# Kernel optimization log

Measured on AMD Instinct MI355X. Metric: run time of the kernel, lower is better.

## Reference

```python
import jax, jax.numpy as jnp
import numpy as np

B, L, D, N = 8, 2048, 1024, 16


def setup_inputs() -> dict:
    key = jax.random.key(0)
    ks = jax.random.split(key, 7)
    x = jax.random.normal(ks[0], (B, L, D), dtype=jnp.float32)
    # A = -rand(d_model, d_state) - 0.5  -> in (-1.5, -0.5)
    A = -jax.random.uniform(ks[1], (D, N), dtype=jnp.float32) - 0.5
    # nn.Linear(d_model, d_state, bias=False): weight [N, D]
    Wb = jax.random.normal(ks[2], (N, D), dtype=jnp.float32) / np.sqrt(D)
    C = jax.random.normal(ks[3], (D, N), dtype=jnp.float32) * 0.1
    Dp = jax.random.normal(ks[4], (D,), dtype=jnp.float32) * 0.1
    # nn.Linear(d_model, d_model): weight [D, D], bias [D]
    Wd = jax.random.normal(ks[5], (D, D), dtype=jnp.float32) / np.sqrt(D)
    bd = jax.random.normal(ks[6], (D,), dtype=jnp.float32) * 0.01
    return {"x": x, "A": A, "Wb": Wb, "C": C, "Dp": Dp, "Wd": Wd, "bd": bd}


def reference(x, A, Wb, C, Dp, Wd, bd):
    # Precompute input-dependent projections for all timesteps (batched GEMMs)
    dt = jax.nn.softplus(jnp.einsum('bld,ed->ble', x, Wd) + bd)  # [B,L,D]
    Bx = jnp.einsum('bld,nd->bln', x, Wb)                        # [B,L,N]

    def step(h, inp):
        dt_t, bx_t, x_t = inp                  # [B,D], [B,N], [B,D]
        dA = dt_t[..., None] * A               # [B,D,N]
        h = jnp.exp(dA) * h + dt_t[..., None] * bx_t[:, None, :]
        y = jnp.einsum('bdn,dn->bd', h, C) + Dp * x_t
        return h, y

    h0 = jnp.zeros((x.shape[0], A.shape[0], A.shape[1]), dtype=x.dtype)
    xs = (jnp.swapaxes(dt, 0, 1), jnp.swapaxes(Bx, 0, 1), jnp.swapaxes(x, 0, 1))
    _, ys = jax.lax.scan(step, h0, xs)         # ys: [L,B,D]
    return jnp.swapaxes(ys, 0, 1)              # [B,L,D]
```

## Files before the change

### kernel.cpp

```cpp
#include <hip/hip_runtime.h>
#include <hip/hip_bf16.h>
#include <stdint.h>

#define B_ 8
#define L_ 2048
#define D_ 1024
#define N_ 16
#define M_ (B_ * L_)
#define K_ D_
#define SEG_ 64
#define SLEN_ (L_ / SEG_)
#define LOG2E 1.44269504088896341f

typedef __bf16 bf16;
typedef __bf16 bf16x8 __attribute__((ext_vector_type(8)));
typedef float f32x4 __attribute__((ext_vector_type(4)));

__global__ __launch_bounds__(256) void cvt_f32_bf16(const float* __restrict__ in,
                                                    bf16* __restrict__ out, int n4) {
  int i = blockIdx.x * 256 + threadIdx.x;
  const int stride = gridDim.x * 256;
  const float4* in4 = (const float4*)in;
  uint2* out2 = (uint2*)out;
  for (; i < n4; i += stride) {
    float4 v = in4[i];
    union { bf16 h[4]; uint2 u; } p;
    p.h[0] = (bf16)v.x; p.h[1] = (bf16)v.y; p.h[2] = (bf16)v.z; p.h[3] = (bf16)v.w;
    out2[i] = p.u;
  }
}

__device__ inline void gload_lds16(const bf16* g, bf16* l) {
  __builtin_amdgcn_global_load_lds(
      (const __attribute__((address_space(1))) void*)g,
      (__attribute__((address_space(3))) void*)l, 16, 0, 0);
}

__device__ inline float softplus_f(float z) {
  return fmaxf(z, 0.f) + __logf(1.f + __expf(-fabsf(z)));
}

__global__ __launch_bounds__(256) void gemm_dt(const bf16* __restrict__ Xb,
                                               const bf16* __restrict__ Wdb,
                                               const float* __restrict__ bd,
                                               bf16* __restrict__ dtb) {
  __shared__ bf16 As[2][128 * 32];
  __shared__ bf16 Bs[2][128 * 32];
  const int tid = threadIdx.x;
  const int lane = tid & 63;
  const int wave = tid >> 6;
  const int wr = wave >> 1, wc = wave & 1;
  const int virt = (blockIdx.x & 7) * 128 + (blockIdx.x >> 3);
  const int mt = virt >> 3, nt = virt & 7;
  const int m0 = mt * 128, n0 = nt * 128;

  const bf16* ga[2];
  const bf16* gb[2];
#pragma unroll
  for (int q = 0; q < 2; ++q) {
    const int c = tid + 256 * q;
    const int row = c >> 2;
    const int col8 = ((c & 3) ^ (row & 3)) * 8;
    ga[q] = Xb + (size_t)(m0 + row) * K_ + col8;
    gb[q] = Wdb + (size_t)(n0 + row) * K_ + col8;
  }

  f32x4 acc[4][4] = {};
  const int frow = (lane & 15);
  const int khalf = (lane >> 4);

  int aoff[4], boff[4];
#pragma unroll
  for (int i = 0; i < 4; ++i) {
    const int Ra = wr * 64 + i * 16 + frow;
    const int Rb = wc * 64 + i * 16 + frow;
    aoff[i] = Ra * 32 + (khalf ^ (Ra & 3)) * 8;
    boff[i] = Rb * 32 + (khalf ^ (Rb & 3)) * 8;
  }

#define STAGE_(buf, kt)                                         \
  {                                                             \
    gload_lds16(ga[0] + (kt), &As[buf][tid * 8]);               \
    gload_lds16(ga[1] + (kt), &As[buf][(tid + 256) * 8]);       \
    gload_lds16(gb[0] + (kt), &Bs[buf][tid * 8]);               \
    gload_lds16(gb[1] + (kt), &Bs[buf][(tid + 256) * 8]);       \
  }

  STAGE_(0, 0);
  __syncthreads();

  int cur = 0;
  for (int t = 0; t < K_ / 32; ++t) {
    if (t + 1 < K_ / 32) STAGE_(cur ^ 1, (t + 1) * 32);
    bf16x8 af[4], bfr[4];
#pragma unroll
    for (int i = 0; i < 4; ++i) af[i] = *(const bf16x8*)&As[cur][aoff[i]];
#pragma unroll
    for (int i = 0; i < 4; ++i) bfr[i] = *(const bf16x8*)&Bs[cur][boff[i]];
#pragma unroll
    for (int i = 0; i < 4; ++i)
#pragma unroll
      for (int j = 0; j < 4; ++j)
        acc[i][j] = __builtin_amdgcn_mfma_f32_16x16x32_bf16(af[i], bfr[j], acc[i][j], 0, 0, 0);
    __syncthreads();
    cur ^= 1;
  }
#undef STAGE_

  const int rbase = m0 + wr * 64 + (lane >> 4) * 4;
  const int cbase = n0 + wc * 64 + (lane & 15);
#pragma unroll
  for (int j = 0; j < 4; ++j) {
    const int col = cbase + j * 16;
    const float bias = bd[col];
#pragma unroll
    for (int i = 0; i < 4; ++i) {
      const int row = rbase + i * 16;
#pragma unroll
      for (int r = 0; r < 4; ++r) {
        float z = acc[i][j][r] + bias;
        dtb[(size_t)(row + r) * D_ + col] = (bf16)softplus_f(z);
      }
    }
  }
}

__global__ __launch_bounds__(256) void bx_mfma(const bf16* __restrict__ Xb,
                                               const bf16* __restrict__ Wbb,
                                               float* __restrict__ Bx) {
  const int lane = threadIdx.x & 63;
  const int wave = threadIdx.x >> 6;
  const int row0 = blockIdx.x * 64 + wave * 16;
  const int fr = lane & 15;
  const int kg = (lane >> 4) * 8;
  const bf16* ga = Xb + (size_t)(row0 + fr) * K_ + kg;
  const bf16* gb = Wbb + (size_t)fr * K_ + kg;
  f32x4 acc = {};
#pragma unroll 8
  for (int kt = 0; kt < K_; kt += 32) {
    bf16x8 af = *(const bf16x8*)(ga + kt);
    bf16x8 bf = *(const bf16x8*)(gb + kt);
    acc = __builtin_amdgcn_mfma_f32_16x16x32_bf16(af, bf, acc, 0, 0, 0);
  }
  const int orow = row0 + (lane >> 4) * 4;
  const int ocol = lane & 15;
#pragma unroll
  for (int r = 0; r < 4; ++r)
    Bx[(size_t)(orow + r) * N_ + ocol] = acc[r];
}

__global__ __launch_bounds__(256) void scan_p1(
    const bf16* __restrict__ dtb, const float* __restrict__ Bx,
    const float* __restrict__ A, bf16* __restrict__ hseg,
    float* __restrict__ stot) {
  const int tid = threadIdx.x;
  const int bi = blockIdx.x;
  const int seg = bi & 63;
  const int dtile = (bi >> 6) & 3;
  const int b = bi >> 8;
  const int d = dtile * 256 + tid;
  const int l0 = seg * SLEN_;

  const float* bxp = Bx + ((size_t)b * L_ + l0) * N_;

  float A2[N_];
  {
    const float4* ap = (const float4*)(A + (size_t)d * N_);
#pragma unroll
    for (int q = 0; q < 4; ++q) {
      float4 a = ap[q];
      A2[q * 4 + 0] = a.x * LOG2E; A2[q * 4 + 1] = a.y * LOG2E;
      A2[q * 4 + 2] = a.z * LOG2E; A2[q * 4 + 3] = a.w * LOG2E;
    }
  }

  const bf16* dtp = dtb + ((size_t)b * L_ + l0) * D_ + d;
  float h[N_] = {};
  float s = 0.f;

  float cdt[4];
#pragma unroll
  for (int u = 0; u < 4; ++u) cdt[u] = (float)dtp[(size_t)u * D_];

#define P1_STEP(i, c0)                                              \
  {                                                                 \
    s += (c0);                                                      \
    _Pragma("unroll")                                               \
    for (int q = 0; q < 4; ++q) {                                   \
      const float4 bv = *(const float4*)(bxp + (i) * N_ + q * 4);   \
      const float bvf[4] = {bv.x, bv.y, bv.z, bv.w};                \
      _Pragma("unroll")                                             \
      for (int j = 0; j < 4; ++j) {                                 \
        const int n = q * 4 + j;                                    \
        const float e = __builtin_amdgcn_exp2f((c0) * A2[n]);       \
        h[n] = fmaf(e, h[n], (c0) * bvf[j]);                        \
      }                                                             \
    }                                                               \
  }

  for (int i0 = 0; i0 < SLEN_ - 4; i0 += 4) {
#pragma unroll
    for (int u = 0; u < 4; ++u) {
      const int i = i0 + u;
      const float c0 = cdt[u];
      cdt[u] = (float)dtp[(size_t)(i + 4) * D_];
      P1_STEP(i, c0);
    }
  }
#pragma unroll
  for (int u = 0; u < 4; ++u) {
    const int i = SLEN_ - 4 + u;
    P1_STEP(i, cdt[u]);
  }
#undef P1_STEP

  bf16* hp = hseg + (((size_t)b * SEG_ + seg) * D_ + d) * N_;
  union { bf16 v[16]; uint4 u[2]; } pk;
#pragma unroll
  for (int n = 0; n < N_; ++n) pk.v[n] = (bf16)h[n];
  ((uint4*)hp)[0] = pk.u[0];
  ((uint4*)hp)[1] = pk.u[1];
  stot[((size_t)b * SEG_ + seg) * D_ + d] = s;
}

__global__ __launch_bounds__(256) void scan_combine(
    const float* __restrict__ A, bf16* __restrict__ hseg,
    const float* __restrict__ stot) {
  const int tid = threadIdx.x;
  const int bi = blockIdx.x;
  const int b = bi >> 6;
  const int d = (bi & 63) * 16 + (tid >> 4);
  const int n = tid & 15;
  const float A2 = A[(size_t)d * N_ + n] * LOG2E;

  const size_t hbase = ((size_t)b * SEG_ * D_ + d) * N_ + n;
  const size_t sbase = (size_t)b * SEG_ * D_ + d;
  float g = 0.f;
  float hs = (float)hseg[hbase];
  float st = stot[sbase];
  for (int sg = 0; sg < SEG_; ++sg) {
    const int s1 = (sg + 1 < SEG_) ? sg + 1 : sg;
    const float nhs = (float)hseg[hbase + (size_t)s1 * D_ * N_];
    const float nst = stot[sbase + (size_t)s1 * D_];
    hseg[hbase + (size_t)sg * D_ * N_] = (bf16)g;
    g = fmaf(__builtin_amdgcn_exp2f(A2 * st), g, hs);
    hs = nhs; st = nst;
  }
}

__global__ __launch_bounds__(256) void scan_p3(
    const bf16* __restrict__ dtb, const float* __restrict__ Bx,
    const bf16* __restrict__ xb, const float* __restrict__ A,
    const float* __restrict__ C, const float* __restrict__ Dp,
    const bf16* __restrict__ hseg, float* __restrict__ out) {
  const int tid = threadIdx.x;
  const int bi = blockIdx.x;
  const int seg = bi & 63;
  const int dtile = (bi >> 6) & 3;
  const int b = bi >> 8;
  const int d = dtile * 256 + tid;
  const int l0 = seg * SLEN_;

  const float* bxp = Bx + ((size_t)b * L_ + l0) * N_;

  float A2[N_], Cv[N_], h[N_];
  {
    const float4* ap = (const float4*)(A + (size_t)d * N_);
    const float4* cp = (const float4*)(C + (size_t)d * N_);
    const bf16* hp = hseg + (((size_t)b * SEG_ + seg) * D_ + d) * N_;
    union { uint4 u[2]; bf16 v[16]; } pk;
    pk.u[0] = ((const uint4*)hp)[0];
    pk.u[1] = ((const uint4*)hp)[1];
#pragma unroll
    for (int q = 0; q < 4; ++q) {
      float4 a = ap[q], c = cp[q];
      A2[q * 4 + 0] = a.x * LOG2E; A2[q * 4 + 1] = a.y * LOG2E;
      A2[q * 4 + 2] = a.z * LOG2E; A2[q * 4 + 3] = a.w * LOG2E;
      Cv[q * 4 + 0] = c.x; Cv[q * 4 + 1] = c.y;
      Cv[q * 4 + 2] = c.z; Cv[q * 4 + 3] = c.w;
    }
#pragma unroll
    for (int n = 0; n < N_; ++n) h[n] = (float)pk.v[n];
  }
  const float Dpv = Dp[d];

  const size_t base = ((size_t)b * L_ + l0) * D_ + d;
  const bf16* dtp = dtb + base;
  const bf16* xp = xb + base;
  float* op = out + base;

  float cdt[2], cx[2];
#pragma unroll
  for (int u = 0; u < 2; ++u) {
    cdt[u] = (float)dtp[(size_t)u * D_];
    cx[u]  = (float)xp[(size_t)u * D_];
  }

#define P3_STEP(i, c0, x0)                                          \
  {                                                                 \
    float y = Dpv * (x0);                                           \
    _Pragma("unroll")                                               \
    for (int q = 0; q < 4; ++q) {                                   \
      const float4 bv = *(const float4*)(bxp + (i) * N_ + q * 4);   \
      const float bvf[4] = {bv.x, bv.y, bv.z, bv.w};                \
      _Pragma("unroll")                                             \
      for (int j = 0; j < 4; ++j) {                                 \
        const int n = q * 4 + j;                                    \
        const float e = __builtin_amdgcn_exp2f((c0) * A2[n]);       \
        h[n] = fmaf(e, h[n], (c0) * bvf[j]);                        \
        y = fmaf(h[n], Cv[n], y);                                   \
      }                                                             \
    }                                                               \
    op[(size_t)(i) * D_] = y;                                       \
  }

  for (int i0 = 0; i0 < SLEN_ - 2; i0 += 2) {
#pragma unroll
    for (int u = 0; u < 2; ++u) {
      const int i = i0 + u;
      const float c0 = cdt[u], x0 = cx[u];
      cdt[u] = (float)dtp[(size_t)(i + 2) * D_];
      cx[u]  = (float)xp[(size_t)(i + 2) * D_];
      P3_STEP(i, c0, x0);
    }
  }
#pragma unroll
  for (int u = 0; u < 2; ++u) {
    const int i = SLEN_ - 2 + u;
    P3_STEP(i, cdt[u], cx[u]);
  }
#undef P3_STEP
}

extern "C" void kernel_launch(void* const* d_in, const int* in_sizes, int n_in,
                              void* d_out, int out_size, void* d_ws, size_t ws_size,
                              hipStream_t stream) {
  const float* x  = (const float*)d_in[0];
  const float* A  = (const float*)d_in[1];
  const float* Wb = (const float*)d_in[2];
  const float* C  = (const float*)d_in[3];
  const float* Dp = (const float*)d_in[4];
  const float* Wd = (const float*)d_in[5];
  const float* bd = (const float*)d_in[6];
  float* out = (float*)d_out;

  char* ws = (char*)d_ws;
  bf16*  dtb  = (bf16*)ws;
  bf16*  xb   = (bf16*)(ws + (size_t)33554432);
  bf16*  wdb  = (bf16*)(ws + (size_t)67108864);
  bf16*  wbb  = (bf16*)(ws + (size_t)69206016);
  float* bx   = (float*)(ws + (size_t)69238784);
  bf16*  hseg = (bf16*)(ws + (size_t)70287360);
  float* stot = (float*)(ws + (size_t)87064576);

  cvt_f32_bf16<<<2048, 256, 0, stream>>>(x, xb, M_ * K_ / 4);
  cvt_f32_bf16<<<1024, 256, 0, stream>>>(Wd, wdb, D_ * K_ / 4);
  cvt_f32_bf16<<<16, 256, 0, stream>>>(Wb, wbb, N_ * K_ / 4);
  bx_mfma<<<dim3(M_ / 64), 256, 0, stream>>>(xb, wbb, bx);
  gemm_dt<<<dim3((M_ / 128) * (D_ / 128)), 256, 0, stream>>>(xb, wdb, bd, dtb);
  scan_p1<<<dim3(B_ * 4 * SEG_), 256, 0, stream>>>(dtb, bx, A, hseg, stot);
  scan_combine<<<dim3(B_ * (D_ / 16)), 256, 0, stream>>>(A, hseg, stot);
  scan_p3<<<dim3(B_ * 4 * SEG_), 256, 0, stream>>>(dtb, bx, xb, A, C, Dp, hseg, out);
}
```

Baseline: 169.4 us.

## Enlarge dt GEMM to 256x256 tiles with phased MFMA/load pipelining

Rewrites the dt projection GEMM to use 256x256 output tiles with 512 threads (8 waves, each 128x64), K-step 64 split into two 32-wide halves, double-buffered LDS staging interleaved between MFMA phases with explicit vmcnt waits, barriers and s_setprio. It aims to raise arithmetic intensity per loaded byte and hide global-to-LDS latency. The cost is far more LDS (128KB), more accumulator registers, and fewer blocks (256), which may leave CUs underfilled on a 256-CU part.

```diff
diff --git a/kernel.cpp b/kernel.cpp
--- a/kernel.cpp
+++ b/kernel.cpp
@@ -40,87 +40,127 @@
   return fmaxf(z, 0.f) + __logf(1.f + __expf(-fabsf(z)));
 }
 
-__global__ __launch_bounds__(256) void gemm_dt(const bf16* __restrict__ Xb,
+__global__ __launch_bounds__(512) void gemm_dt(const bf16* __restrict__ Xb,
                                                const bf16* __restrict__ Wdb,
                                                const float* __restrict__ bd,
                                                bf16* __restrict__ dtb) {
-  __shared__ bf16 As[2][128 * 32];
-  __shared__ bf16 Bs[2][128 * 32];
+  __shared__ bf16 SA[2][2][256 * 32];
+  __shared__ bf16 SB[2][2][256 * 32];
   const int tid = threadIdx.x;
   const int lane = tid & 63;
   const int wave = tid >> 6;
-  const int wr = wave >> 1, wc = wave & 1;
-  const int virt = (blockIdx.x & 7) * 128 + (blockIdx.x >> 3);
-  const int mt = virt >> 3, nt = virt & 7;
-  const int m0 = mt * 128, n0 = nt * 128;
-
-  const bf16* ga[2];
-  const bf16* gb[2];
+  const int wr = wave >> 2;
+  const int wc = wave & 3;
+  const int virt = (blockIdx.x & 7) * 32 + (blockIdx.x >> 3);
+  const int mt = virt >> 2, nt = virt & 3;
+  const int m0 = mt * 256, n0 = nt * 256;
+
+  const bf16* gA[2];
+  const bf16* gB[2];
+  int ldst[2];
 #pragma unroll
   for (int q = 0; q < 2; ++q) {
-    const int c = tid + 256 * q;
-    const int row = c >> 2;
-    const int col8 = ((c & 3) ^ (row & 3)) * 8;
-    ga[q] = Xb + (size_t)(m0 + row) * K_ + col8;
-    gb[q] = Wdb + (size_t)(n0 + row) * K_ + col8;
-  }
-
-  f32x4 acc[4][4] = {};
-  const int frow = (lane & 15);
-  const int khalf = (lane >> 4);
-
-  int aoff[4], boff[4];
-#pragma unroll
-  for (int i = 0; i < 4; ++i) {
-    const int Ra = wr * 64 + i * 16 + frow;
-    const int Rb = wc * 64 + i * 16 + frow;
-    aoff[i] = Ra * 32 + (khalf ^ (Ra & 3)) * 8;
-    boff[i] = Rb * 32 + (khalf ^ (Rb & 3)) * 8;
-  }
-
-#define STAGE_(buf, kt)                                         \
-  {                                                             \
-    gload_lds16(ga[0] + (kt), &As[buf][tid * 8]);               \
-    gload_lds16(ga[1] + (kt), &As[buf][(tid + 256) * 8]);       \
-    gload_lds16(gb[0] + (kt), &Bs[buf][tid * 8]);               \
-    gload_lds16(gb[1] + (kt), &Bs[buf][(tid + 256) * 8]);       \
-  }
-
-  STAGE_(0, 0);
-  __syncthreads();
-
-  int cur = 0;
-  for (int t = 0; t < K_ / 32; ++t) {
-    if (t + 1 < K_ / 32) STAGE_(cur ^ 1, (t + 1) * 32);
-    bf16x8 af[4], bfr[4];
-#pragma unroll
-    for (int i = 0; i < 4; ++i) af[i] = *(const bf16x8*)&As[cur][aoff[i]];
-#pragma unroll
-    for (int i = 0; i < 4; ++i) bfr[i] = *(const bf16x8*)&Bs[cur][boff[i]];
-#pragma unroll
-    for (int i = 0; i < 4; ++i)
-#pragma unroll
-      for (int j = 0; j < 4; ++j)
-        acc[i][j] = __builtin_amdgcn_mfma_f32_16x16x32_bf16(af[i], bfr[j], acc[i][j], 0, 0, 0);
-    __syncthreads();
-    cur ^= 1;
-  }
-#undef STAGE_
-
-  const int rbase = m0 + wr * 64 + (lane >> 4) * 4;
-  const int cbase = n0 + wc * 64 + (lane & 15);
+    const int cc = tid + 512 * q;
+    const int row = cc >> 2, c = cc & 3;
+    const int sk = (c ^ ((row >> 1) & 3)) * 8;
+    gA[q] = Xb + (size_t)(m0 + row) * K_ + sk;
+    gB[q] = Wdb + (size_t)(n0 + row) * K_ + sk;
+    ldst[q] = cc * 8;
+  }
+
+#define STA(bf_, kh_, kt_)                                              \
+  { gload_lds16(gA[0] + (kt_) * 64 + (kh_) * 32, &SA[bf_][kh_][ldst[0]]); \
+    gload_lds16(gA[1] + (kt_) * 64 + (kh_) * 32, &SA[bf_][kh_][ldst[1]]); }
+#define STB(bf_, kh_, kt_)                                              \
+  { gload_lds16(gB[0] + (kt_) * 64 + (kh_) * 32, &SB[bf_][kh_][ldst[0]]); \
+    gload_lds16(gB[1] + (kt_) * 64 + (kh_) * 32, &SB[bf_][kh_][ldst[1]]); }
+
+  const int fr = lane & 15;
+  const int kq = lane >> 4;
+  int aoff[8], boff[4];
+#pragma unroll
+  for (int i = 0; i < 8; ++i) {
+    const int R = wr * 128 + i * 16 + fr;
+    aoff[i] = R * 32 + ((kq ^ ((R >> 1) & 3)) * 8);
+  }
 #pragma unroll
   for (int j = 0; j < 4; ++j) {
-    const int col = cbase + j * 16;
+    const int R = wc * 64 + j * 16 + fr;
+    boff[j] = R * 32 + ((kq ^ ((R >> 1) & 3)) * 8);
+  }
+
+  f32x4 acc[8][4] = {};
+  bf16x8 a[8];
+
+#define MF(d_, av_, bv_) d_ = __builtin_amdgcn_mfma_f32_16x16x32_bf16(av_, bv_, d_, 0, 0, 0)
+
+#define PH_A(bf_, kh_)                                                  \
+  {                                                                     \
+    _Pragma("unroll")                                                   \
+    for (int i = 0; i < 8; ++i) a[i] = *(const bf16x8*)&SA[bf_][kh_][aoff[i]]; \
+    bf16x8 b0 = *(const bf16x8*)&SB[bf_][kh_][boff[0]];                 \
+    bf16x8 b1 = *(const bf16x8*)&SB[bf_][kh_][boff[1]];                 \
+    __builtin_amdgcn_s_setprio(1);                                      \
+    _Pragma("unroll")                                                   \
+    for (int i = 0; i < 8; ++i) { MF(acc[i][0], a[i], b0); MF(acc[i][1], a[i], b1); } \
+    __builtin_amdgcn_s_setprio(0);                                      \
+    __builtin_amdgcn_s_barrier();                                       \
+  }
+#define PH_B(bf_, kh_)                                                  \
+  {                                                                     \
+    bf16x8 b2 = *(const bf16x8*)&SB[bf_][kh_][boff[2]];                 \
+    bf16x8 b3 = *(const bf16x8*)&SB[bf_][kh_][boff[3]];                 \
+    __builtin_amdgcn_s_setprio(1);                                      \
+    _Pragma("unroll")                                                   \
+    for (int i = 0; i < 8; ++i) { MF(acc[i][2], a[i], b2); MF(acc[i][3], a[i], b3); } \
+    __builtin_amdgcn_s_setprio(0);                                      \
+    __builtin_amdgcn_s_barrier();                                       \
+  }
+
+#define TILE(bf_, nb_, t_, STG_)                                        \
+  {                                                                     \
+    if (STG_) { STA(nb_, 0, (t_) + 1); }                                \
+    if (STG_) { asm volatile("s_waitcnt vmcnt(6)" ::: "memory"); }      \
+    else      { asm volatile("s_waitcnt vmcnt(4)" ::: "memory"); }      \
+    __builtin_amdgcn_s_barrier();                                       \
+    PH_A(bf_, 0)                                                        \
+    if (STG_) { STB(nb_, 0, (t_) + 1); }                                \
+    PH_B(bf_, 0)                                                        \
+    if (STG_) { STA(nb_, 1, (t_) + 1); }                                \
+    if (STG_) { asm volatile("s_waitcnt vmcnt(6)" ::: "memory"); }      \
+    else      { asm volatile("s_waitcnt vmcnt(0)" ::: "memory"); }      \
+    __builtin_amdgcn_s_barrier();                                       \
+    PH_A(bf_, 1)                                                        \
+    if (STG_) { STB(nb_, 1, (t_) + 1); }                                \
+    PH_B(bf_, 1)                                                        \
+  }
+
+  STA(0, 0, 0); STB(0, 0, 0); STA(0, 1, 0); STB(0, 1, 0);
+
+#pragma unroll 1
+  for (int t2 = 0; t2 < 8; ++t2) {
+    TILE(0, 1, 2 * t2, true)
+    TILE(1, 0, 2 * t2 + 1, (t2 < 7))
+  }
+#undef TILE
+#undef PH_A
+#undef PH_B
+#undef MF
+#undef STA
+#undef STB
+
+  const int rb = m0 + wr * 128 + (lane >> 4) * 4;
+  const int cb = n0 + wc * 64 + (lane & 15);
+#pragma unroll
+  for (int j = 0; j < 4; ++j) {
+    const int col = cb + j * 16;
     const float bias = bd[col];
 #pragma unroll
-    for (int i = 0; i < 4; ++i) {
-      const int row = rbase + i * 16;
-#pragma unroll
-      for (int r = 0; r < 4; ++r) {
-        float z = acc[i][j][r] + bias;
-        dtb[(size_t)(row + r) * D_ + col] = (bf16)softplus_f(z);
-      }
+    for (int i = 0; i < 8; ++i) {
+      const int row = rb + i * 16;
+#pragma unroll
+      for (int r = 0; r < 4; ++r)
+        dtb[(size_t)(row + r) * D_ + col] = (bf16)softplus_f(acc[i][j][r] + bias);
     }
   }
 }
@@ -357,7 +397,7 @@
   cvt_f32_bf16<<<1024, 256, 0, stream>>>(Wd, wdb, D_ * K_ / 4);
   cvt_f32_bf16<<<16, 256, 0, stream>>>(Wb, wbb, N_ * K_ / 4);
   bx_mfma<<<dim3(M_ / 64), 256, 0, stream>>>(xb, wbb, bx);
-  gemm_dt<<<dim3((M_ / 128) * (D_ / 128)), 256, 0, stream>>>(xb, wdb, bd, dtb);
+  gemm_dt<<<dim3((M_ / 256) * (D_ / 256)), 512, 0, stream>>>(xb, wdb, bd, dtb);
   scan_p1<<<dim3(B_ * 4 * SEG_), 256, 0, stream>>>(dtb, bx, A, hseg, stot);
   scan_combine<<<dim3(B_ * (D_ / 16)), 256, 0, stream>>>(A, hseg, stot);
   scan_p3<<<dim3(B_ * 4 * SEG_), 256, 0, stream>>>(dtb, bx, xb, A, C, Dp, hseg, out);
```

After: 167.6 us. No clear change (-1.0%).

## Split each channel's state dimension across two half-waves in scan kernels

Applied to the files above, without the earlier changes.

The segmented scan kernels now assign each d channel to two lanes, with each lane owning 8 of the 16 state entries. This doubles the grid, halves per-thread serial work and registers, and gives more parallelism to hide exp and FMA latency. In exchange, dt/x loads are duplicated across the two halves, the output sum needs a cross-lane shuffle, and half the lanes are idle on stores.

```diff
diff --git a/kernel.cpp b/kernel.cpp
--- a/kernel.cpp
+++ b/kernel.cpp
@@ -156,18 +156,21 @@
   const int tid = threadIdx.x;
   const int bi = blockIdx.x;
   const int seg = bi & 63;
-  const int dtile = (bi >> 6) & 3;
-  const int b = bi >> 8;
-  const int d = dtile * 256 + tid;
+  const int dtile = (bi >> 6) & 7;
+  const int b = bi >> 9;
+  const int lane = tid & 63;
+  const int wave = tid >> 6;
+  const int half = lane >> 5;
+  const int d = dtile * 128 + wave * 32 + (lane & 31);
   const int l0 = seg * SLEN_;
 
-  const float* bxp = Bx + ((size_t)b * L_ + l0) * N_;
-
-  float A2[N_];
+  const float* bxp = Bx + ((size_t)b * L_ + l0) * N_ + half * 8;
+
+  float A2[8];
   {
-    const float4* ap = (const float4*)(A + (size_t)d * N_);
-#pragma unroll
-    for (int q = 0; q < 4; ++q) {
+    const float4* ap = (const float4*)(A + (size_t)d * N_ + half * 8);
+#pragma unroll
+    for (int q = 0; q < 2; ++q) {
       float4 a = ap[q];
       A2[q * 4 + 0] = a.x * LOG2E; A2[q * 4 + 1] = a.y * LOG2E;
       A2[q * 4 + 2] = a.z * LOG2E; A2[q * 4 + 3] = a.w * LOG2E;
@@ -175,18 +178,18 @@
   }
 
   const bf16* dtp = dtb + ((size_t)b * L_ + l0) * D_ + d;
-  float h[N_] = {};
+  float h[8] = {};
   float s = 0.f;
 
-  float cdt[4];
-#pragma unroll
-  for (int u = 0; u < 4; ++u) cdt[u] = (float)dtp[(size_t)u * D_];
+  float cdt[2];
+#pragma unroll
+  for (int u = 0; u < 2; ++u) cdt[u] = (float)dtp[(size_t)u * D_];
 
 #define P1_STEP(i, c0)                                              \
   {                                                                 \
     s += (c0);                                                      \
     _Pragma("unroll")                                               \
-    for (int q = 0; q < 4; ++q) {                                   \
+    for (int q = 0; q < 2; ++q) {                                   \
       const float4 bv = *(const float4*)(bxp + (i) * N_ + q * 4);   \
       const float bvf[4] = {bv.x, bv.y, bv.z, bv.w};                \
       _Pragma("unroll")                                             \
@@ -198,29 +201,28 @@
     }                                                               \
   }
 
-  for (int i0 = 0; i0 < SLEN_ - 4; i0 += 4) {
-#pragma unroll
-    for (int u = 0; u < 4; ++u) {
+  for (int i0 = 0; i0 < SLEN_ - 2; i0 += 2) {
+#pragma unroll
+    for (int u = 0; u < 2; ++u) {
       const int i = i0 + u;
       const float c0 = cdt[u];
-      cdt[u] = (float)dtp[(size_t)(i + 4) * D_];
+      cdt[u] = (float)dtp[(size_t)(i + 2) * D_];
       P1_STEP(i, c0);
     }
   }
 #pragma unroll
-  for (int u = 0; u < 4; ++u) {
-    const int i = SLEN_ - 4 + u;
+  for (int u = 0; u < 2; ++u) {
+    const int i = SLEN_ - 2 + u;
     P1_STEP(i, cdt[u]);
   }
 #undef P1_STEP
 
-  bf16* hp = hseg + (((size_t)b * SEG_ + seg) * D_ + d) * N_;
-  union { bf16 v[16]; uint4 u[2]; } pk;
-#pragma unroll
-  for (int n = 0; n < N_; ++n) pk.v[n] = (bf16)h[n];
-  ((uint4*)hp)[0] = pk.u[0];
-  ((uint4*)hp)[1] = pk.u[1];
-  stot[((size_t)b * SEG_ + seg) * D_ + d] = s;
+  bf16* hp = hseg + (((size_t)b * SEG_ + seg) * D_ + d) * N_ + half * 8;
+  union { bf16 v[8]; uint4 u; } pk;
+#pragma unroll
+  for (int n = 0; n < 8; ++n) pk.v[n] = (bf16)h[n];
+  *(uint4*)hp = pk.u;
+  if (half == 0) stot[((size_t)b * SEG_ + seg) * D_ + d] = s;
 }
 
 __global__ __launch_bounds__(256) void scan_combine(
@@ -256,23 +258,25 @@
   const int tid = threadIdx.x;
   const int bi = blockIdx.x;
   const int seg = bi & 63;
-  const int dtile = (bi >> 6) & 3;
-  const int b = bi >> 8;
-  const int d = dtile * 256 + tid;
+  const int dtile = (bi >> 6) & 7;
+  const int b = bi >> 9;
+  const int lane = tid & 63;
+  const int wave = tid >> 6;
+  const int half = lane >> 5;
+  const int d = dtile * 128 + wave * 32 + (lane & 31);
   const int l0 = seg * SLEN_;
 
-  const float* bxp = Bx + ((size_t)b * L_ + l0) * N_;
-
-  float A2[N_], Cv[N_], h[N_];
+  const float* bxp = Bx + ((size_t)b * L_ + l0) * N_ + half * 8;
+
+  float A2[8], Cv[8], h[8];
   {
-    const float4* ap = (const float4*)(A + (size_t)d * N_);
-    const float4* cp = (const float4*)(C + (size_t)d * N_);
-    const bf16* hp = hseg + (((size_t)b * SEG_ + seg) * D_ + d) * N_;
-    union { uint4 u[2]; bf16 v[16]; } pk;
-    pk.u[0] = ((const uint4*)hp)[0];
-    pk.u[1] = ((const uint4*)hp)[1];
-#pragma unroll
-    for (int q = 0; q < 4; ++q) {
+    const float4* ap = (const float4*)(A + (size_t)d * N_ + half * 8);
+    const float4* cp = (const float4*)(C + (size_t)d * N_ + half * 8);
+    const bf16* hp = hseg + (((size_t)b * SEG_ + seg) * D_ + d) * N_ + half * 8;
+    union { uint4 u; bf16 v[8]; } pk;
+    pk.u = *(const uint4*)hp;
+#pragma unroll
+    for (int q = 0; q < 2; ++q) {
       float4 a = ap[q], c = cp[q];
       A2[q * 4 + 0] = a.x * LOG2E; A2[q * 4 + 1] = a.y * LOG2E;
       A2[q * 4 + 2] = a.z * LOG2E; A2[q * 4 + 3] = a.w * LOG2E;
@@ -280,9 +284,9 @@
       Cv[q * 4 + 2] = c.z; Cv[q * 4 + 3] = c.w;
     }
 #pragma unroll
-    for (int n = 0; n < N_; ++n) h[n] = (float)pk.v[n];
-  }
-  const float Dpv = Dp[d];
+    for (int n = 0; n < 8; ++n) h[n] = (float)pk.v[n];
+  }
+  const float Dpv = (half == 0) ? Dp[d] : 0.f;
 
   const size_t base = ((size_t)b * L_ + l0) * D_ + d;
   const bf16* dtp = dtb + base;
@@ -300,7 +304,7 @@
   {                                                                 \
     float y = Dpv * (x0);                                           \
     _Pragma("unroll")                                               \
-    for (int q = 0; q < 4; ++q) {                                   \
+    for (int q = 0; q < 2; ++q) {                                   \
       const float4 bv = *(const float4*)(bxp + (i) * N_ + q * 4);   \
       const float bvf[4] = {bv.x, bv.y, bv.z, bv.w};                \
       _Pragma("unroll")                                             \
@@ -311,7 +315,8 @@
         y = fmaf(h[n], Cv[n], y);                                   \
       }                                                             \
     }                                                               \
-    op[(size_t)(i) * D_] = y;                                       \
+    y += __shfl_xor(y, 32);                                         \
+    if (half == 0) op[(size_t)(i) * D_] = y;                        \
   }
 
   for (int i0 = 0; i0 < SLEN_ - 2; i0 += 2) {
@@ -358,7 +363,7 @@
   cvt_f32_bf16<<<16, 256, 0, stream>>>(Wb, wbb, N_ * K_ / 4);
   bx_mfma<<<dim3(M_ / 64), 256, 0, stream>>>(xb, wbb, bx);
   gemm_dt<<<dim3((M_ / 128) * (D_ / 128)), 256, 0, stream>>>(xb, wdb, bd, dtb);
-  scan_p1<<<dim3(B_ * 4 * SEG_), 256, 0, stream>>>(dtb, bx, A, hseg, stot);
+  scan_p1<<<dim3(B_ * 8 * SEG_), 256, 0, stream>>>(dtb, bx, A, hseg, stot);
   scan_combine<<<dim3(B_ * (D_ / 16)), 256, 0, stream>>>(A, hseg, stot);
-  scan_p3<<<dim3(B_ * 4 * SEG_), 256, 0, stream>>>(dtb, bx, xb, A, C, Dp, hseg, out);
-}
+  scan_p3<<<dim3(B_ * 8 * SEG_), 256, 0, stream>>>(dtb, bx, xb, A, C, Dp, hseg, out);
+}
```

Result: slower. 182.2 us (+7.6%).
